# Performance work log

Measured on AMD Instinct MI355X. Metric: run time of the kernel, lower is better.

Reference implementation:

```python
import jax, jax.numpy as jnp
import numpy as np

H = 256          # lstm_size
VOCAB = 6        # num_branches + 1
NBR = 5          # num_branches
TEMP = 5.0
OP_TANH = 1.1 / 2.5
BLOCKS, SEQ = 16, 2048


def setup_inputs() -> dict:
    key = jax.random.key(0)
    ks = jax.random.split(key, 12)
    def gw(k, shape, scale=0.05):
        return jax.random.normal(k, shape, dtype=jnp.float32) * scale
    return {
        "arc": jax.random.randint(ks[0], (BLOCKS, SEQ), 0, VOCAB, dtype=jnp.int32),
        "h0": gw(ks[1], (2, 1, H), 0.01),
        "c0": gw(ks[2], (2, 1, H), 0.01),
        "emb": gw(ks[3], (VOCAB, H)),
        "Wih_f": gw(ks[4], (4 * H, H)), "Whh_f": gw(ks[5], (4 * H, H)),
        "bih_f": jnp.zeros(4 * H, jnp.float32), "bhh_f": jnp.zeros(4 * H, jnp.float32),
        "Wih_b": gw(ks[6], (4 * H, H)), "Whh_b": gw(ks[7], (4 * H, H)),
        "bih_b": jnp.zeros(4 * H, jnp.float32), "bhh_b": jnp.zeros(4 * H, jnp.float32),
        "fcW": gw(ks[8], (NBR, 2 * H)), "fcb": jnp.zeros(NBR, jnp.float32),
    }


def _lstm_dir(x, h0, c0, Wih, Whh, bih, bhh):
    # x: [T,H]; one direction of a 1-layer LSTM, PyTorch gate order (i,f,g,o)
    def step(carry, xt):
        h, c = carry
        g = xt @ Wih.T + h @ Whh.T + bih + bhh          # [4H]
        i, f, gg, o = jnp.split(g, 4)
        i, f, o = jax.nn.sigmoid(i), jax.nn.sigmoid(f), jax.nn.sigmoid(o)
        c = f * c + i * jnp.tanh(gg)
        h = o * jnp.tanh(c)
        return (h, c), h
    (hT, cT), hs = jax.lax.scan(step, (h0, c0), x)
    return hs, hT, cT


def reference(arc, h0, c0, emb, Wih_f, Whh_f, bih_f, bhh_f,
              Wih_b, Whh_b, bih_b, bhh_b, fcW, fcb):
    key0 = jax.random.key(42)

    def block(carry, arc_i):
        hf, cf, hb, cb, key = carry
        key, sub = jax.random.split(key)
        x = emb[arc_i]                                   # [T,H]
        hs_f, hfT, cfT = _lstm_dir(x, hf, cf, Wih_f, Whh_f, bih_f, bhh_f)
        hs_b, hbT, cbT = _lstm_dir(x[::-1], hb, cb, Wih_b, Whh_b, bih_b, bhh_b)
        out = jnp.concatenate([hs_f, hs_b[::-1]], axis=-1)   # [T,2H]
        logits = (out @ fcW.T + fcb) / TEMP
        logits = OP_TANH * jnp.tanh(logits)              # [T,5]
        logp = jax.nn.log_softmax(logits, axis=-1)
        prob = jnp.exp(logp)
        idx = jax.random.categorical(sub, logits, axis=-1)   # multinomial(softmax(logits))
        # F.cross_entropy(logits, idx) == mean NLL of sampled indices
        ce = -jnp.mean(jnp.take_along_axis(logp, idx[:, None], axis=-1))
        # original: -mean(sum(logp*prob over size-1 dim)) == -mean over [T,5]
        ent = jax.lax.stop_gradient(-jnp.mean(logp * prob))
        return (hfT, cfT, hbT, cbT, key), (idx, ce, ent)

    init = (h0[0, 0], c0[0, 0], h0[1, 0], c0[1, 0], key0)
    (hfT, cfT, hbT, cbT, _), (all_arc, ces, ents) = jax.lax.scan(block, init, arc)
    h = jnp.stack([hfT, hbT])[:, None, :]                # [2,1,H]
    c = jnp.stack([cfT, cbT])[:, None, :]
    return all_arc, jnp.sum(ces), jnp.sum(ents), h, c
```

## Files before the change

### kernel.cpp

```cpp
#include <hip/hip_runtime.h>
#include <math.h>
#include <stdint.h>

static constexpr int XG_OFF   = 0;
static constexpr int MB_OFF   = 12288;
static constexpr int SH_OFF   = 20480;
static constexpr int SC_OFF   = 20992;
static constexpr int HIST_OFF = 21504;
static constexpr int HIST_D   = 524288;
static constexpr int CEP_OFF  = 1070080;
static constexpr int ENTP_OFF = 1070144;

static constexpr int OUT_CE = 32768;
static constexpr int OUT_H  = 32770;
static constexpr int OUT_C  = 33282;

__device__ __forceinline__ uint32_t rotl32(uint32_t v, int n) {
  return (v << n) | (v >> (32 - n));
}
__device__ __forceinline__ void tf2x32(uint32_t k0, uint32_t k1,
                                       uint32_t x0, uint32_t x1,
                                       uint32_t& y0, uint32_t& y1) {
  const uint32_t k2 = k0 ^ k1 ^ 0x1BD11BDAu;
  x0 += k0; x1 += k1;
  x0 += x1; x1 = rotl32(x1, 13); x1 ^= x0;
  x0 += x1; x1 = rotl32(x1, 15); x1 ^= x0;
  x0 += x1; x1 = rotl32(x1, 26); x1 ^= x0;
  x0 += x1; x1 = rotl32(x1, 6);  x1 ^= x0;
  x0 += k1; x1 += k2 + 1u;
  x0 += x1; x1 = rotl32(x1, 17); x1 ^= x0;
  x0 += x1; x1 = rotl32(x1, 29); x1 ^= x0;
  x0 += x1; x1 = rotl32(x1, 16); x1 ^= x0;
  x0 += x1; x1 = rotl32(x1, 24); x1 ^= x0;
  x0 += k2; x1 += k0 + 2u;
  x0 += x1; x1 = rotl32(x1, 13); x1 ^= x0;
  x0 += x1; x1 = rotl32(x1, 15); x1 ^= x0;
  x0 += x1; x1 = rotl32(x1, 26); x1 ^= x0;
  x0 += x1; x1 = rotl32(x1, 6);  x1 ^= x0;
  x0 += k0; x1 += k1 + 3u;
  x0 += x1; x1 = rotl32(x1, 17); x1 ^= x0;
  x0 += x1; x1 = rotl32(x1, 29); x1 ^= x0;
  x0 += x1; x1 = rotl32(x1, 16); x1 ^= x0;
  x0 += x1; x1 = rotl32(x1, 24); x1 ^= x0;
  x0 += k1; x1 += k2 + 4u;
  x0 += x1; x1 = rotl32(x1, 13); x1 ^= x0;
  x0 += x1; x1 = rotl32(x1, 15); x1 ^= x0;
  x0 += x1; x1 = rotl32(x1, 26); x1 ^= x0;
  x0 += x1; x1 = rotl32(x1, 6);  x1 ^= x0;
  x0 += k2; x1 += k0 + 5u;
  y0 = x0; y1 = x1;
}

__device__ __forceinline__ float gumbel_from_bits(uint32_t bits) {
  float f = __uint_as_float(0x3f800000u | (bits >> 9)) - 1.0f;
  const float tiny = __uint_as_float(0x00800000u);
  float u = fmaxf(tiny, f + tiny);
  float l1 = (float)log((double)u);
  return -(float)log(-(double)l1);
}

__global__ void k_xg(const float* __restrict__ emb,
                     const float* __restrict__ WihF, const float* __restrict__ bihF,
                     const float* __restrict__ bhhF,
                     const float* __restrict__ WihB, const float* __restrict__ bihB,
                     const float* __restrict__ bhhB,
                     float* __restrict__ ws) {
  __shared__ float se[1536];
  const int tid = threadIdx.x;
  for (int i = tid; i < 1536; i += 256) se[i] = emb[i];
  __syncthreads();
  const int gid = blockIdx.x * 256 + tid;
  const int d = gid >> 10, r = gid & 1023;
  const float* Wih = d ? WihB : WihF;
  const float* bih = d ? bihB : bihF;
  const float* bhh = d ? bhhB : bhhF;
  float acc[6] = {0.f, 0.f, 0.f, 0.f, 0.f, 0.f};
  const float4* wr = (const float4*)(Wih + r * 256);
  for (int c = 0; c < 64; c++) {
    float4 wv = wr[c];
#pragma unroll
    for (int v = 0; v < 6; v++) {
      const float* ev = &se[v * 256 + 4 * c];
      acc[v] += wv.x * ev[0] + wv.y * ev[1] + wv.z * ev[2] + wv.w * ev[3];
    }
  }
  const float bsum = bih[r] + bhh[r];
#pragma unroll
  for (int v = 0; v < 6; v++) ws[XG_OFF + d * 6144 + v * 1024 + r] = acc[v] + bsum;
}

__global__ __launch_bounds__(256, 1)
void k_chain(const int* __restrict__ arc, const float* __restrict__ h0,
             const float* __restrict__ c0, const float* __restrict__ WhhF,
             const float* __restrict__ WhhB, float* __restrict__ ws,
             float* __restrict__ out, int b) {
  const int tid = threadIdx.x;
  const int d = blockIdx.x >> 3;
  const int k = blockIdx.x & 7;
  const int w = tid >> 6;
  const int lane = tid & 63;
  const int q = lane >> 4, p = lane & 15;

  __shared__ float xg_l[768];
  __shared__ int arc_s[2048];
  __shared__ float h_s[2][256];

  const float* Whh = d ? WhhB : WhhF;
  for (int i = tid; i < 768; i += 256) {
    const int sym = i >> 7, r = i & 127, el = r >> 2, g = r & 3;
    xg_l[i] = ws[XG_OFF + d * 6144 + sym * 1024 + g * 256 + 32 * k + el];
  }
  {
    const int* ab = arc + b * 2048;
    for (int i = tid; i < 2048; i += 256) arc_s[i] = ab[i];
  }
  const int eA = 32 * k + 8 * w + 2 * q;
  const int elA = 8 * w + 2 * q;
  float4 W[8][4];
#pragma unroll
  for (int i = 0; i < 8; i++) {
    const int R = 256 * (i >> 1) + eA + (i & 1);
    const float* rp = Whh + R * 256 + 16 * p;
#pragma unroll
    for (int j = 0; j < 4; j++) W[i][j] = ((const float4*)rp)[j];
  }
  h_s[0][tid] = (b == 0) ? h0[d * 256 + tid] : ws[SH_OFF + d * 256 + tid];
  float cA = (b == 0) ? c0[d * 256 + eA] : ws[SC_OFF + d * 256 + eA];
  float cB = (b == 0) ? c0[d * 256 + eA + 1] : ws[SC_OFF + d * 256 + eA + 1];
  float hA = 0.f, hB = 0.f;
  __syncthreads();
  float4 hw[4];
  {
    const float4* hp = (const float4*)&h_s[0][16 * p];
#pragma unroll
    for (int j = 0; j < 4; j++) hw[j] = hp[j];
  }
  unsigned long long* mb = (unsigned long long*)(ws + MB_OFF);
  const unsigned stampBase = (unsigned)b * 2048u;
  float* histD = ws + HIST_OFF + d * HIST_D;
  const bool selfPoll = ((tid >> 5) == k);

  for (int t = 0; t < 2048; t++) {
    float acc[8];
#pragma unroll
    for (int i = 0; i < 8; i++) {
      float a;
      a  = W[i][0].x * hw[0].x;
      a += W[i][0].y * hw[0].y;
      a += W[i][0].z * hw[0].z;
      a += W[i][0].w * hw[0].w;
      a += W[i][1].x * hw[1].x;
      a += W[i][1].y * hw[1].y;
      a += W[i][1].z * hw[1].z;
      a += W[i][1].w * hw[1].w;
      a += W[i][2].x * hw[2].x;
      a += W[i][2].y * hw[2].y;
      a += W[i][2].z * hw[2].z;
      a += W[i][2].w * hw[2].w;
      a += W[i][3].x * hw[3].x;
      a += W[i][3].y * hw[3].y;
      a += W[i][3].z * hw[3].z;
      a += W[i][3].w * hw[3].w;
      acc[i] = a;
    }
#pragma unroll
    for (int i = 0; i < 8; i++) {
      float v = acc[i];
      v += __shfl_xor(v, 1, 16);
      v += __shfl_xor(v, 2, 16);
      v += __shfl_xor(v, 4, 16);
      v += __shfl_xor(v, 8, 16);
      acc[i] = v;
    }
    const int sym = arc_s[d ? (2047 - t) : t];
    const float4 xgA = *(const float4*)&xg_l[sym * 128 + elA * 4];
    const float4 xgB = *(const float4*)&xg_l[sym * 128 + elA * 4 + 4];
    {
      const float gi = acc[0] + xgA.x;
      const float gf = acc[2] + xgA.y;
      const float gg = acc[4] + xgA.z;
      const float go = acc[6] + xgA.w;
      const float I = 1.0f / (1.0f + expf(-gi));
      const float F = 1.0f / (1.0f + expf(-gf));
      const float G = tanhf(gg);
      const float O = 1.0f / (1.0f + expf(-go));
      cA = F * cA + I * G;
      hA = O * tanhf(cA);
    }
    {
      const float gi = acc[1] + xgB.x;
      const float gf = acc[3] + xgB.y;
      const float gg = acc[5] + xgB.z;
      const float go = acc[7] + xgB.w;
      const float I = 1.0f / (1.0f + expf(-gi));
      const float F = 1.0f / (1.0f + expf(-gf));
      const float G = tanhf(gg);
      const float O = 1.0f / (1.0f + expf(-go));
      cB = F * cB + I * G;
      hB = O * tanhf(cB);
    }
    const unsigned stamp = stampBase + (unsigned)t + 1u;
    unsigned long long* mbp = mb + (d * 2 + (t & 1)) * 256;
    const int np = (t + 1) & 1;
    if (p < 2) {
      const int e = eA + p;
      const float hv = p ? hB : hA;
      const unsigned long long pk = (unsigned long long)__float_as_uint(hv) |
                                    ((unsigned long long)stamp << 32);
      __hip_atomic_store(&mbp[e], pk, __ATOMIC_RELAXED, __HIP_MEMORY_SCOPE_AGENT);
      histD[t * 256 + e] = hv;
      h_s[np][e] = hv;
    }
    asm volatile("s_waitcnt vmcnt(0)" ::: "memory");
    if (!selfPoll) {
      unsigned long long v;
      for (;;) {
        unsigned long long v0 = __hip_atomic_load(&mbp[tid], __ATOMIC_RELAXED,
                                                  __HIP_MEMORY_SCOPE_AGENT);
        unsigned long long v1 = __hip_atomic_load(&mbp[tid], __ATOMIC_RELAXED,
                                                  __HIP_MEMORY_SCOPE_AGENT);
        if ((unsigned)(v0 >> 32) == stamp) { v = v0; break; }
        if ((unsigned)(v1 >> 32) == stamp) { v = v1; break; }
      }
      h_s[np][tid] = __uint_as_float((unsigned)v);
    }
    __syncthreads();
    {
      const float4* hp = (const float4*)&h_s[np][16 * p];
#pragma unroll
      for (int j = 0; j < 4; j++) hw[j] = hp[j];
    }
  }

  if (p < 2) {
    const int e = eA + p;
    ws[SH_OFF + d * 256 + e] = p ? hB : hA;
    ws[SC_OFF + d * 256 + e] = p ? cB : cA;
    if (b == 15) {
      out[OUT_H + d * 256 + e] = p ? hB : hA;
      out[OUT_C + d * 256 + e] = p ? cB : cA;
    }
  }
}

__global__ void k_sampler(const float* __restrict__ fcW, const float* __restrict__ fcb,
                          float* __restrict__ ws, float* __restrict__ out, int b) {
  const int tid = threadIdx.x;
  __shared__ float sW[5 * 512];
  __shared__ float sb[5];
  __shared__ float red[256];
  for (int i = tid; i < 2560; i += 256) sW[i] = fcW[i];
  if (tid < 5) sb[tid] = fcb[tid];
  __syncthreads();
  uint32_t s0 = 0u, s1 = 0u;
  {
    uint32_t k0 = 0u, k1 = 42u;
    for (int i = 0; i <= b; i++) {
      uint32_t n0, n1, t0, t1;
      tf2x32(k0, k1, 0u, 0u, n0, n1);
      tf2x32(k0, k1, 0u, 1u, t0, t1);
      s0 = t0; s1 = t1;
      k0 = n0; k1 = n1;
    }
  }
  const int pp = blockIdx.x * 256 + tid;
  const float* histF = ws + HIST_OFF;
  const float* histB = ws + HIST_OFF + HIST_D;
  float dotL[5] = {0.f, 0.f, 0.f, 0.f, 0.f};
  float dotH[5] = {0.f, 0.f, 0.f, 0.f, 0.f};
  const float4* hfL = (const float4*)(histF + pp * 256);
  const float4* hbL = (const float4*)(histB + (2047 - pp) * 256);
  const float4* hfH = (const float4*)(histF + (pp + 1024) * 256);
  const float4* hbH = (const float4*)(histB + (1023 - pp) * 256);
  for (int c = 0; c < 64; c++) {
    float4 a = hfL[c], bb = hbL[c], e = hfH[c], f = hbH[c];
#pragma unroll
    for (int j = 0; j < 5; j++) {
      const float* wr = &sW[j * 512 + 4 * c];
      dotL[j] += a.x * wr[0] + a.y * wr[1] + a.z * wr[2] + a.w * wr[3];
      dotL[j] += bb.x * wr[256] + bb.y * wr[257] + bb.z * wr[258] + bb.w * wr[259];
      dotH[j] += e.x * wr[0] + e.y * wr[1] + e.z * wr[2] + e.w * wr[3];
      dotH[j] += f.x * wr[256] + f.y * wr[257] + f.z * wr[258] + f.w * wr[259];
    }
  }
  uint32_t bl[5], bh[5];
#pragma unroll
  for (int j = 0; j < 5; j++) {
    uint32_t y0, y1;
    tf2x32(s0, s1, 0u, (uint32_t)(5 * pp + j), y0, y1);
    bl[j] = y0 ^ y1;
    tf2x32(s0, s1, 0u, (uint32_t)(5 * (pp + 1024) + j), y0, y1);
    bh[j] = y0 ^ y1;
  }
  const float OPT = (float)(1.1 / 2.5);
  float ce_acc = 0.f, ent_acc = 0.f;
#pragma unroll
  for (int half = 0; half < 2; half++) {
    const int t = half ? (pp + 1024) : pp;
    float l[5];
#pragma unroll
    for (int j = 0; j < 5; j++) {
      float dv = half ? dotH[j] : dotL[j];
      l[j] = OPT * tanhf((dv + sb[j]) / 5.0f);
    }
    int idx = 0;
    float best;
    {
      uint32_t b0 = half ? bh[0] : bl[0];
      best = gumbel_from_bits(b0) + l[0];
    }
#pragma unroll
    for (int j = 1; j < 5; j++) {
      uint32_t bj = half ? bh[j] : bl[j];
      float v = gumbel_from_bits(bj) + l[j];
      if (v > best) { best = v; idx = j; }
    }
    out[b * 2048 + t] = (float)idx;
    float m = l[0];
#pragma unroll
    for (int j = 1; j < 5; j++) m = fmaxf(m, l[j]);
    float ssum = 0.f;
#pragma unroll
    for (int j = 0; j < 5; j++) ssum += expf(l[j] - m);
    float lse = logf(ssum);
    float lpidx = 0.f;
#pragma unroll
    for (int j = 0; j < 5; j++) {
      float lp = (l[j] - m) - lse;
      ent_acc -= lp * expf(lp);
      lpidx = (j == idx) ? lp : lpidx;
    }
    ce_acc -= lpidx;
  }
  red[tid] = ce_acc; __syncthreads();
  for (int s = 128; s > 0; s >>= 1) {
    if (tid < s) red[tid] += red[tid + s];
    __syncthreads();
  }
  if (tid == 0) ws[CEP_OFF + b * 4 + blockIdx.x] = red[0];
  __syncthreads();
  red[tid] = ent_acc; __syncthreads();
  for (int s = 128; s > 0; s >>= 1) {
    if (tid < s) red[tid] += red[tid + s];
    __syncthreads();
  }
  if (tid == 0) ws[ENTP_OFF + b * 4 + blockIdx.x] = red[0];
}

__global__ void k_final(const float* __restrict__ ws, float* __restrict__ out) {
  if (threadIdx.x == 0 && blockIdx.x == 0) {
    float ce = 0.f, ent = 0.f;
    for (int b = 0; b < 16; b++) {
      float cb = 0.f, eb = 0.f;
      for (int j = 0; j < 4; j++) {
        cb += ws[CEP_OFF + b * 4 + j];
        eb += ws[ENTP_OFF + b * 4 + j];
      }
      ce += cb / 2048.0f;
      ent += eb / 10240.0f;
    }
    out[OUT_CE] = ce;
    out[OUT_CE + 1] = ent;
  }
}

extern "C" void kernel_launch(void* const* d_in, const int* in_sizes, int n_in,
                              void* d_out, int out_size, void* d_ws, size_t ws_size,
                              hipStream_t stream) {
  (void)in_sizes; (void)n_in; (void)out_size; (void)ws_size;
  const int* arc = (const int*)d_in[0];
  const float* h0 = (const float*)d_in[1];
  const float* c0 = (const float*)d_in[2];
  const float* emb = (const float*)d_in[3];
  const float* WihF = (const float*)d_in[4];
  const float* WhhF = (const float*)d_in[5];
  const float* bihF = (const float*)d_in[6];
  const float* bhhF = (const float*)d_in[7];
  const float* WihB = (const float*)d_in[8];
  const float* WhhB = (const float*)d_in[9];
  const float* bihB = (const float*)d_in[10];
  const float* bhhB = (const float*)d_in[11];
  const float* fcW = (const float*)d_in[12];
  const float* fcb = (const float*)d_in[13];
  float* out = (float*)d_out;
  float* ws = (float*)d_ws;

  hipLaunchKernelGGL(k_xg, dim3(8), dim3(256), 0, stream,
                     emb, WihF, bihF, bhhF, WihB, bihB, bhhB, ws);
  for (int b = 0; b < 16; b++) {
    hipLaunchKernelGGL(k_chain, dim3(16), dim3(256), 0, stream,
                       arc, h0, c0, WhhF, WhhB, ws, out, b);
    hipLaunchKernelGGL(k_sampler, dim3(4), dim3(256), 0, stream,
                       fcW, fcb, ws, out, b);
  }
  hipLaunchKernelGGL(k_final, dim3(1), dim3(64), 0, stream, ws, out);
}
```

Baseline: 69.58 ms.

## Poll mailbox directly into registers, dropping shared-memory h exchange and block barrier

Each thread now polls the 16 mailbox entries it needs straight from global memory into its h-vector registers. This replaces the old scheme, where each thread polled one entry, wrote it to shared memory, and the block synchronised with __syncthreads before rereading. The goal is to remove the per-step block barrier and the LDS round trip from the serial recurrence critical path. The trade-offs are 16x more atomic loads per thread while spinning (more L2 traffic), and mailbox parity is now keyed on the global stamp rather than t. A lane with p==0 now writes both outputs, and the last step skips the poll.

```diff
diff --git a/kernel.cpp b/kernel.cpp
--- a/kernel.cpp
+++ b/kernel.cpp
@@ -103,7 +103,6 @@
 
   __shared__ float xg_l[768];
   __shared__ int arc_s[2048];
-  __shared__ float h_s[2][256];
 
   const float* Whh = d ? WhhB : WhhF;
   for (int i = tid; i < 768; i += 256) {
@@ -124,21 +123,18 @@
 #pragma unroll
     for (int j = 0; j < 4; j++) W[i][j] = ((const float4*)rp)[j];
   }
-  h_s[0][tid] = (b == 0) ? h0[d * 256 + tid] : ws[SH_OFF + d * 256 + tid];
+  const float* hprev = (b == 0) ? (h0 + d * 256) : (ws + SH_OFF + d * 256);
+  float4 hw[4];
+#pragma unroll
+  for (int j = 0; j < 4; j++) hw[j] = ((const float4*)(hprev + 16 * p))[j];
   float cA = (b == 0) ? c0[d * 256 + eA] : ws[SC_OFF + d * 256 + eA];
   float cB = (b == 0) ? c0[d * 256 + eA + 1] : ws[SC_OFF + d * 256 + eA + 1];
   float hA = 0.f, hB = 0.f;
   __syncthreads();
-  float4 hw[4];
-  {
-    const float4* hp = (const float4*)&h_s[0][16 * p];
-#pragma unroll
-    for (int j = 0; j < 4; j++) hw[j] = hp[j];
-  }
+
   unsigned long long* mb = (unsigned long long*)(ws + MB_OFF);
   const unsigned stampBase = (unsigned)b * 2048u;
   float* histD = ws + HIST_OFF + d * HIST_D;
-  const bool selfPoll = ((tid >> 5) == k);
 
   for (int t = 0; t < 2048; t++) {
     float acc[8];
@@ -199,46 +195,48 @@
       cB = F * cB + I * G;
       hB = O * tanhf(cB);
     }
-    const unsigned stamp = stampBase + (unsigned)t + 1u;
-    unsigned long long* mbp = mb + (d * 2 + (t & 1)) * 256;
-    const int np = (t + 1) & 1;
-    if (p < 2) {
-      const int e = eA + p;
-      const float hv = p ? hB : hA;
-      const unsigned long long pk = (unsigned long long)__float_as_uint(hv) |
-                                    ((unsigned long long)stamp << 32);
-      __hip_atomic_store(&mbp[e], pk, __ATOMIC_RELAXED, __HIP_MEMORY_SCOPE_AGENT);
-      histD[t * 256 + e] = hv;
-      h_s[np][e] = hv;
-    }
-    asm volatile("s_waitcnt vmcnt(0)" ::: "memory");
-    if (!selfPoll) {
-      unsigned long long v;
-      for (;;) {
-        unsigned long long v0 = __hip_atomic_load(&mbp[tid], __ATOMIC_RELAXED,
-                                                  __HIP_MEMORY_SCOPE_AGENT);
-        unsigned long long v1 = __hip_atomic_load(&mbp[tid], __ATOMIC_RELAXED,
-                                                  __HIP_MEMORY_SCOPE_AGENT);
-        if ((unsigned)(v0 >> 32) == stamp) { v = v0; break; }
-        if ((unsigned)(v1 >> 32) == stamp) { v = v1; break; }
-      }
-      h_s[np][tid] = __uint_as_float((unsigned)v);
-    }
-    __syncthreads();
-    {
-      const float4* hp = (const float4*)&h_s[np][16 * p];
-#pragma unroll
-      for (int j = 0; j < 4; j++) hw[j] = hp[j];
-    }
-  }
-
-  if (p < 2) {
-    const int e = eA + p;
-    ws[SH_OFF + d * 256 + e] = p ? hB : hA;
-    ws[SC_OFF + d * 256 + e] = p ? cB : cA;
+    const unsigned S = stampBase + (unsigned)t + 1u;
+    unsigned long long* mbp = mb + (d * 2 + (int)(S & 1u)) * 256;
+    if (p == 0) {
+      const unsigned long long pkA = (unsigned long long)__float_as_uint(hA) |
+                                     ((unsigned long long)S << 32);
+      const unsigned long long pkB = (unsigned long long)__float_as_uint(hB) |
+                                     ((unsigned long long)S << 32);
+      __hip_atomic_store(&mbp[eA], pkA, __ATOMIC_RELAXED, __HIP_MEMORY_SCOPE_AGENT);
+      __hip_atomic_store(&mbp[eA + 1], pkB, __ATOMIC_RELAXED, __HIP_MEMORY_SCOPE_AGENT);
+      *(float2*)&histD[t * 256 + eA] = make_float2(hA, hB);
+    }
+    if (t == 2047) break;
+    const unsigned long long* src = mbp + 16 * p;
+    unsigned long long e[16];
+    for (;;) {
+#pragma unroll
+      for (int j = 0; j < 16; j++)
+        e[j] = __hip_atomic_load(&src[j], __ATOMIC_RELAXED, __HIP_MEMORY_SCOPE_AGENT);
+      bool ok = true;
+#pragma unroll
+      for (int j = 0; j < 16; j++) ok &= ((unsigned)(e[j] >> 32) == S);
+      if (ok) break;
+    }
+#pragma unroll
+    for (int j = 0; j < 4; j++) {
+      hw[j].x = __uint_as_float((unsigned)e[4 * j + 0]);
+      hw[j].y = __uint_as_float((unsigned)e[4 * j + 1]);
+      hw[j].z = __uint_as_float((unsigned)e[4 * j + 2]);
+      hw[j].w = __uint_as_float((unsigned)e[4 * j + 3]);
+    }
+  }
+
+  if (p == 0) {
+    ws[SH_OFF + d * 256 + eA] = hA;
+    ws[SH_OFF + d * 256 + eA + 1] = hB;
+    ws[SC_OFF + d * 256 + eA] = cA;
+    ws[SC_OFF + d * 256 + eA + 1] = cB;
     if (b == 15) {
-      out[OUT_H + d * 256 + e] = p ? hB : hA;
-      out[OUT_C + d * 256 + e] = p ? cB : cA;
+      out[OUT_H + d * 256 + eA] = hA;
+      out[OUT_H + d * 256 + eA + 1] = hB;
+      out[OUT_C + d * 256 + eA] = cA;
+      out[OUT_C + d * 256 + eA + 1] = cB;
     }
   }
 }
```

Result: slower. 141.9 ms (+104.0%).

## Elect chain workgroups on a single XCD and poll mailboxes through L2

Applied to the files above, without the earlier changes.

The chain kernel now launches 128 workgroups. Each reads its XCC id and takes a ticket on a per-XCC atomic counter. The first XCC to collect 16 workgroups wins the election, and only those 16 run the recurrence, so all cross-workgroup exchange of h stays within one XCD's L2. The mailbox is duplicated: one copy is written and polled with sc0 loads and stores for fast intra-XCD visibility, and the other is an agent-scope fallback that takes over after repeated timeouts. Also reads the initial h straight from global memory, pads the shared h buffer to avoid bank conflicts, and skips the final exchange. The cost is an extra zeroing kernel per block, election overhead, and reliance on XCC co-residency that could deadlock if 16 workgroups never land on one XCD.

```diff
diff --git a/kernel.cpp b/kernel.cpp
--- a/kernel.cpp
+++ b/kernel.cpp
@@ -3,7 +3,9 @@
 #include <stdint.h>
 
 static constexpr int XG_OFF   = 0;
-static constexpr int MB_OFF   = 12288;
+static constexpr int MBA_OFF  = 12288;
+static constexpr int MBB_OFF  = 14336;
+static constexpr int ELEC_OFF = 16384;
 static constexpr int SH_OFF   = 20480;
 static constexpr int SC_OFF   = 20992;
 static constexpr int HIST_OFF = 21504;
@@ -14,6 +16,16 @@
 static constexpr int OUT_CE = 32768;
 static constexpr int OUT_H  = 32770;
 static constexpr int OUT_C  = 33282;
+
+__device__ __forceinline__ void st_sc0(unsigned long long* p, unsigned long long v) {
+  asm volatile("global_store_dwordx2 %0, %1, off sc0" :: "v"(p), "v"(v) : "memory");
+}
+__device__ __forceinline__ unsigned long long ld_sc0(const unsigned long long* p) {
+  unsigned long long r;
+  asm volatile("global_load_dwordx2 %0, %1, off sc0\n\ts_waitcnt vmcnt(0)"
+               : "=&v"(r) : "v"(p) : "memory");
+  return r;
+}
 
 __device__ __forceinline__ uint32_t rotl32(uint32_t v, int n) {
   return (v << n) | (v >> (32 - n));
@@ -89,21 +101,49 @@
   for (int v = 0; v < 6; v++) ws[XG_OFF + d * 6144 + v * 1024 + r] = acc[v] + bsum;
 }
 
+__global__ void k_zero(float* __restrict__ ws) {
+  if (threadIdx.x < 16) ((int*)(ws + ELEC_OFF))[threadIdx.x] = 0;
+}
+
 __global__ __launch_bounds__(256, 1)
 void k_chain(const int* __restrict__ arc, const float* __restrict__ h0,
              const float* __restrict__ c0, const float* __restrict__ WhhF,
              const float* __restrict__ WhhB, float* __restrict__ ws,
              float* __restrict__ out, int b) {
   const int tid = threadIdx.x;
-  const int d = blockIdx.x >> 3;
-  const int k = blockIdx.x & 7;
+  __shared__ int role_s;
+  __shared__ float xg_l[768];
+  __shared__ int arc_s[2048];
+  __shared__ float h_s[2][320];
+
+  if (tid == 0) {
+    int xcc;
+    asm volatile("s_getreg_b32 %0, hwreg(HW_REG_XCC_ID)" : "=s"(xcc));
+    xcc &= 7;
+    int* cnt = (int*)(ws + ELEC_OFF);
+    int* winner = cnt + 8;
+    int pos = __hip_atomic_fetch_add(&cnt[xcc], 1, __ATOMIC_RELAXED,
+                                     __HIP_MEMORY_SCOPE_AGENT);
+    if (pos == 15) {
+      int expected = 0;
+      __hip_atomic_compare_exchange_strong(winner, &expected, xcc + 1,
+          __ATOMIC_RELAXED, __ATOMIC_RELAXED, __HIP_MEMORY_SCOPE_AGENT);
+    }
+    int wv;
+    do {
+      wv = __hip_atomic_load(winner, __ATOMIC_RELAXED, __HIP_MEMORY_SCOPE_AGENT);
+    } while (wv == 0);
+    role_s = (pos < 16 && wv == xcc + 1) ? pos : -1;
+  }
+  __syncthreads();
+  const int role = role_s;
+  if (role < 0) return;
+
+  const int d = role >> 3;
+  const int k = role & 7;
   const int w = tid >> 6;
   const int lane = tid & 63;
   const int q = lane >> 4, p = lane & 15;
-
-  __shared__ float xg_l[768];
-  __shared__ int arc_s[2048];
-  __shared__ float h_s[2][256];
 
   const float* Whh = d ? WhhB : WhhF;
   for (int i = tid; i < 768; i += 256) {
@@ -124,21 +164,21 @@
 #pragma unroll
     for (int j = 0; j < 4; j++) W[i][j] = ((const float4*)rp)[j];
   }
-  h_s[0][tid] = (b == 0) ? h0[d * 256 + tid] : ws[SH_OFF + d * 256 + tid];
+  const float* hprev = (b == 0) ? (h0 + d * 256) : (ws + SH_OFF + d * 256);
+  float4 hw[4];
+#pragma unroll
+  for (int j = 0; j < 4; j++) hw[j] = ((const float4*)(hprev + 16 * p))[j];
   float cA = (b == 0) ? c0[d * 256 + eA] : ws[SC_OFF + d * 256 + eA];
   float cB = (b == 0) ? c0[d * 256 + eA + 1] : ws[SC_OFF + d * 256 + eA + 1];
   float hA = 0.f, hB = 0.f;
   __syncthreads();
-  float4 hw[4];
-  {
-    const float4* hp = (const float4*)&h_s[0][16 * p];
-#pragma unroll
-    for (int j = 0; j < 4; j++) hw[j] = hp[j];
-  }
-  unsigned long long* mb = (unsigned long long*)(ws + MB_OFF);
+
+  unsigned long long* mbA = (unsigned long long*)(ws + MBA_OFF);
+  unsigned long long* mbB = (unsigned long long*)(ws + MBB_OFF);
   const unsigned stampBase = (unsigned)b * 2048u;
   float* histD = ws + HIST_OFF + d * HIST_D;
   const bool selfPoll = ((tid >> 5) == k);
+  int lim = 24, fails = 0;
 
   for (int t = 0; t < 2048; t++) {
     float acc[8];
@@ -199,34 +239,47 @@
       cB = F * cB + I * G;
       hB = O * tanhf(cB);
     }
-    const unsigned stamp = stampBase + (unsigned)t + 1u;
-    unsigned long long* mbp = mb + (d * 2 + (t & 1)) * 256;
+    const unsigned S = stampBase + (unsigned)t + 1u;
+    const int mbo = (d * 2 + (t & 1)) * 256;
+    unsigned long long* mbAp = mbA + mbo;
+    unsigned long long* mbBp = mbB + mbo;
     const int np = (t + 1) & 1;
     if (p < 2) {
       const int e = eA + p;
       const float hv = p ? hB : hA;
       const unsigned long long pk = (unsigned long long)__float_as_uint(hv) |
-                                    ((unsigned long long)stamp << 32);
-      __hip_atomic_store(&mbp[e], pk, __ATOMIC_RELAXED, __HIP_MEMORY_SCOPE_AGENT);
+                                    ((unsigned long long)S << 32);
+      __hip_atomic_store(&mbBp[e], pk, __ATOMIC_RELAXED, __HIP_MEMORY_SCOPE_AGENT);
+      st_sc0(&mbAp[e], pk);
       histD[t * 256 + e] = hv;
-      h_s[np][e] = hv;
+      h_s[np][(e >> 4) * 20 + (e & 15)] = hv;
     }
     asm volatile("s_waitcnt vmcnt(0)" ::: "memory");
-    if (!selfPoll) {
-      unsigned long long v;
-      for (;;) {
-        unsigned long long v0 = __hip_atomic_load(&mbp[tid], __ATOMIC_RELAXED,
-                                                  __HIP_MEMORY_SCOPE_AGENT);
-        unsigned long long v1 = __hip_atomic_load(&mbp[tid], __ATOMIC_RELAXED,
-                                                  __HIP_MEMORY_SCOPE_AGENT);
-        if ((unsigned)(v0 >> 32) == stamp) { v = v0; break; }
-        if ((unsigned)(v1 >> 32) == stamp) { v = v1; break; }
+    if (t == 2047) break;
+    {
+      unsigned long long v = 0;
+      bool got = false;
+      for (int it = 0; it < lim; ++it) {
+        unsigned long long f = selfPoll ? 0ull : ld_sc0(&mbAp[tid]);
+        bool ok = selfPoll | ((unsigned)(f >> 32) == S);
+        if (__all(ok)) { v = f; got = true; break; }
       }
-      h_s[np][tid] = __uint_as_float((unsigned)v);
+      if (!got) {
+        if (++fails >= 4) lim = 0;
+        for (;;) {
+          unsigned long long f = selfPoll ? 0ull :
+              __hip_atomic_load(&mbBp[tid], __ATOMIC_RELAXED,
+                                __HIP_MEMORY_SCOPE_AGENT);
+          bool ok = selfPoll | ((unsigned)(f >> 32) == S);
+          if (__all(ok)) { v = f; break; }
+        }
+      }
+      if (!selfPoll)
+        h_s[np][(tid >> 4) * 20 + (tid & 15)] = __uint_as_float((unsigned)v);
     }
     __syncthreads();
     {
-      const float4* hp = (const float4*)&h_s[np][16 * p];
+      const float4* hp = (const float4*)&h_s[np][20 * p];
 #pragma unroll
       for (int j = 0; j < 4; j++) hw[j] = hp[j];
     }
@@ -388,7 +441,8 @@
   hipLaunchKernelGGL(k_xg, dim3(8), dim3(256), 0, stream,
                      emb, WihF, bihF, bhhF, WihB, bihB, bhhB, ws);
   for (int b = 0; b < 16; b++) {
-    hipLaunchKernelGGL(k_chain, dim3(16), dim3(256), 0, stream,
+    hipLaunchKernelGGL(k_zero, dim3(1), dim3(64), 0, stream, ws);
+    hipLaunchKernelGGL(k_chain, dim3(128), dim3(256), 0, stream,
                        arc, h0, c0, WhhF, WhhB, ws, out, b);
     hipLaunchKernelGGL(k_sampler, dim3(4), dim3(256), 0, stream,
                        fcW, fcb, ws, out, b);
```

Result: faster. 64.72 ms (-7.0%).
